# Kernel tuning notes

Hardware: AMD Instinct MI355X
Metric: run time of the kernel (lower is better)

The kernel has to match this reference:

```python
import jax, jax.numpy as jnp
import numpy as np

B, S, M, KD, VD, QD, H, NQ = 256, 200, 32, 128, 256, 128, 64, 10000
TA, TB, TC = 0.075, 0.088, 1.0  # triangular membership params a, b, c


def setup_inputs() -> dict:
    key = jax.random.key(0)
    ks = jax.random.split(key, 12)
    q_data = jax.random.randint(ks[0], (B, S), 0, NQ + 1)
    # kaiming-normal-ish embedding table; padding_idx=0 row zeroed
    q_embed_weight = jax.random.normal(ks[1], (NQ + 1, QD)) * np.sqrt(2.0 / QD)
    q_embed_weight = q_embed_weight.at[0].set(0.0)
    key_mem = jax.random.normal(ks[2], (M, KD)) * np.sqrt(2.0 / KD)
    value_mem = jax.random.normal(ks[3], (M, VD)) * np.sqrt(2.0 / VD)
    in_dim = VD + QD
    s = 1.0 / np.sqrt(H)
    W_ih = jax.random.uniform(ks[4], (4 * H, in_dim), minval=-s, maxval=s)
    W_hh = jax.random.uniform(ks[5], (4 * H, H), minval=-s, maxval=s)
    b_ih = jax.random.uniform(ks[6], (4 * H,), minval=-s, maxval=s)
    b_hh = jax.random.uniform(ks[7], (4 * H,), minval=-s, maxval=s)
    W_pred = jax.random.normal(ks[8], (1, H)) * np.sqrt(2.0 / H)
    b_pred = jnp.zeros((1,))
    init_h = jax.random.normal(ks[9], (B, H))
    init_c = jax.random.normal(ks[10], (B, H))
    return dict(q_data=q_data, q_embed_weight=q_embed_weight, key_mem=key_mem,
                value_mem=value_mem, W_ih=W_ih, W_hh=W_hh, b_ih=b_ih, b_hh=b_hh,
                W_pred=W_pred, b_pred=b_pred, init_h=init_h, init_c=init_c)


def triangular_layer(cw):
    """cw: [N, M] correlation weights -> [N] unique-row indices.
    Faithful to torch: trit-quantize each weight {0,1,2}, then map each row to its
    index in the (lexicographically sorted) unique-row table, which is exactly what
    the pairwise squared-distance matmul + (dist==0).nonzero() trick computes."""
    w = jnp.minimum((cw - TA) / (TB - TA), (TC - cw) / (TC - TB))
    w = jnp.maximum(w, 0.0)
    iv = jnp.where(w >= 0.6, 2, jnp.where(w >= 0.1, 1, 0)).astype(jnp.int32)  # [N, M]
    # pack 32 trits into two int32 keys (3^16 < 2^31)
    p = jnp.power(3, jnp.arange(16, dtype=jnp.int32))  # [16]
    kh = (iv[:, :16] * p).sum(1)
    kl = (iv[:, 16:] * p).sum(1)
    order = jnp.lexsort((kl, kh))  # primary key kh
    kh_s, kl_s = kh[order], kl[order]
    change = jnp.concatenate([jnp.zeros((1,), jnp.int32),
                              ((kh_s[1:] != kh_s[:-1]) | (kl_s[1:] != kl_s[:-1])).astype(jnp.int32)])
    rank_sorted = jnp.cumsum(change)
    inv = jnp.zeros(cw.shape[0], jnp.int32).at[order].set(rank_sorted)
    return inv


def reference(q_data, q_embed_weight, key_mem, value_mem, W_ih, W_hh, b_ih, b_hh,
              W_pred, b_pred, init_h, init_c):
    q_emb = q_embed_weight[q_data]                                  # [B,S,QD]
    cw = jax.nn.softmax(jnp.einsum('bsd,md->bsm', q_emb, key_mem))  # DKVMN attention
    read = jnp.einsum('bsm,mv->bsv', cw, value_mem)                 # [B,S,VD]
    ids = triangular_layer(cw.reshape(B * S, M))                    # [B*S]
    x = jnp.concatenate([read, q_emb], axis=-1)                     # [B,S,VD+QD]

    def step(carry, xt):
        h, c = carry
        g = xt @ W_ih.T + h @ W_hh.T + b_ih + b_hh
        i, f, gg, o = jnp.split(g, 4, axis=-1)
        c = jax.nn.sigmoid(f) * c + jax.nn.sigmoid(i) * jnp.tanh(gg)
        h = jax.nn.sigmoid(o) * jnp.tanh(c)
        return (h, c), h

    _, hs = jax.lax.scan(step, (init_h, init_c), jnp.swapaxes(x, 0, 1))
    hs = jnp.swapaxes(hs, 0, 1)                                     # [B,S,H]
    pred = jax.nn.sigmoid(hs @ W_pred.T + b_pred)[..., 0]           # [B,S]
    return pred, ids
```

## Files before the change

kernel.cpp:

```cpp
#include <hip/hip_runtime.h>

#define BB 256
#define SS 200
#define MM 32
#define KDIM 128
#define VDIM 256
#define QDIM 128
#define HH 64
#define NROWS 10001
#define NSAMP (BB*SS)
#define INDIM (VDIM+QDIM)
#define DHS 8192
#define DHMASK (DHS-1)
#define XR 16
#define NB_ATTN 2501

typedef unsigned long long u64;
typedef unsigned int u32;
typedef float f16v __attribute__((ext_vector_type(16)));

__device__ __forceinline__ float fexp(float x){ return __builtin_amdgcn_exp2f(x * 1.44269504f); }
__device__ __forceinline__ float fsigm(float x){ return __builtin_amdgcn_rcpf(1.f + fexp(-x)); }
__device__ __forceinline__ float ftanh(float x){ return 1.f - 2.f*__builtin_amdgcn_rcpf(1.f + fexp(2.f*x)); }
__device__ __forceinline__ int clampq(int q){ return q < 0 ? 0 : (q > NROWS-1 ? NROWS-1 : q); }

__device__ __forceinline__ u32 hash64(u64 x){
  x ^= x >> 33; x *= 0xff51afd7ed558ccdULL;
  x ^= x >> 33; x *= 0xc4ceb9fe1a85ec53ULL;
  x ^= x >> 33;
  return (u32)x;
}

__device__ __forceinline__ u64 shflx64(u64 v, int m){
  int lo = __shfl_xor((int)(u32)v, m, 64);
  int hi = __shfl_xor((int)(u32)(v >> 32), m, 64);
  return ((u64)(u32)hi << 32) | (u32)lo;
}

__global__ void k_tr(const float* __restrict__ W_ih, const float* __restrict__ key_mem,
                     float* __restrict__ WQT4, float* __restrict__ KT,
                     float* __restrict__ WVT, u32* __restrict__ present){
  int idx = blockIdx.x*256 + threadIdx.x;
  if (idx < 131072) {
    int dd = idx & 3, j = (idx >> 2) & 255, d4 = idx >> 10;
    WQT4[idx] = W_ih[j*INDIM + VDIM + 4*d4 + dd];
  } else if (idx < 135168) {
    int t = idx - 131072;
    int m = t & 31, d = t >> 5; KT[t] = key_mem[m*KDIM + d];
  } else if (idx < 200704) {
    int t = idx - 135168;
    int j = t & 255, v = t >> 8; WVT[v*256 + j] = W_ih[j*INDIM + v];
  } else {
    int t = idx - 200704;
    if (t < NROWS) present[t] = 0u;
  }
}

__global__ __launch_bounds__(256) void k_front(
    const float* __restrict__ emb, const float* __restrict__ KT,
    const float* __restrict__ val, const float* __restrict__ WVT,
    const int* __restrict__ q_data,
    float* __restrict__ CW, u64* __restrict__ KEYT,
    float* __restrict__ VW, u32* __restrict__ present){
  int bid = blockIdx.x;
  if (bid < NB_ATTN) {
    int w = threadIdx.x >> 6, l = threadIdx.x & 63;
    int n = bid*4 + w;
    __shared__ float se[4][QDIM];
    bool valid = (n < NROWS);
    if (valid) {
      se[w][l]      = emb[n*QDIM + l];
      se[w][l + 64] = emb[n*QDIM + l + 64];
    }
    __syncthreads();
    int m = l & 31;
    float logit = 0.f;
    if (valid && l < 32)
      for (int d = 0; d < KDIM; ++d) logit += se[w][d] * KT[d*32 + m];
    float mx = logit;
    #pragma unroll
    for (int msk = 16; msk >= 1; msk >>= 1) mx = fmaxf(mx, __shfl_xor(mx, msk, 64));
    float e = (l < 32) ? expf(logit - mx) : 0.f;
    float sum = e;
    #pragma unroll
    for (int msk = 16; msk >= 1; msk >>= 1) sum += __shfl_xor(sum, msk, 64);
    float cw = e / sum;
    float wv = fminf((cw - 0.075f)/0.013f, (1.0f - cw)/0.912f);
    wv = fmaxf(wv, 0.f);
    int iv = (wv >= 0.6f) ? 2 : ((wv >= 0.1f) ? 1 : 0);
    int ee = (m < 16) ? m + 16 : m - 16;
    u64 p3 = 1;
    for (int i = 0; i < 31; ++i) if (i < ee) p3 *= 3ULL;
    u64 term = (valid && l < 32) ? (u64)iv * p3 : 0ULL;
    #pragma unroll
    for (int msk = 16; msk >= 1; msk >>= 1) term += shflx64(term, msk);
    if (valid && l < 32) CW[n*256 + m] = cw;
    if (valid && l == 0) KEYT[n] = term;
  } else if (bid < NB_ATTN + MM) {
    int m = bid - NB_ATTN, j = threadIdx.x;
    __shared__ float sval[VDIM];
    sval[j] = val[m*VDIM + j];
    __syncthreads();
    float a0=0.f, a1=0.f, a2=0.f, a3=0.f;
    for (int v = 0; v < VDIM; v += 4) {
      a0 += sval[v+0]*WVT[(v+0)*256 + j];
      a1 += sval[v+1]*WVT[(v+1)*256 + j];
      a2 += sval[v+2]*WVT[(v+2)*256 + j];
      a3 += sval[v+3]*WVT[(v+3)*256 + j];
    }
    VW[m*256 + j] = (a0+a1)+(a2+a3);
  } else {
    int i = (bid - NB_ATTN - MM)*256 + threadIdx.x;
    if (i < NSAMP) present[clampq(q_data[i])] = 1u;
  }
}

__global__ __launch_bounds__(256) void k_xw(
    const float* __restrict__ CW, const float* __restrict__ emb,
    const float* __restrict__ VW, const float* __restrict__ WQT4,
    const float* __restrict__ b_ih, const float* __restrict__ b_hh,
    float* __restrict__ XW4){
  int base = blockIdx.x * XR;
  int j = threadIdx.x;
  __shared__ float scw[XR][32];
  __shared__ __align__(16) float ses[XR][QDIM];
  for (int idx = j; idx < XR*32; idx += 256) {
    int r = idx >> 5, m = idx & 31, n = base + r;
    scw[r][m] = (n < NROWS) ? CW[n*256 + m] : 0.f;
  }
  for (int idx = j; idx < XR*QDIM; idx += 256) {
    int r = idx >> 7, d = idx & 127, n = base + r;
    ses[r][d] = (n < NROWS) ? emb[n*QDIM + d] : 0.f;
  }
  __syncthreads();
  float bias = b_ih[j] + b_hh[j];
  float acc[XR];
  #pragma unroll
  for (int r = 0; r < XR; ++r) acc[r] = bias;
  for (int m = 0; m < MM; ++m) {
    float wv = VW[m*256 + j];
    #pragma unroll
    for (int r = 0; r < XR; ++r) acc[r] += scw[r][m] * wv;
  }
  for (int d4 = 0; d4 < QDIM/4; ++d4) {
    float4 wq = *(const float4*)(WQT4 + d4*1024 + j*4);
    #pragma unroll
    for (int r = 0; r < XR; ++r) {
      float4 ev = *(const float4*)(&ses[r][4*d4]);
      acc[r] += ev.x*wq.x + ev.y*wq.y + ev.z*wq.z + ev.w*wq.w;
    }
  }
  int gate = j >> 6, unit = j & 63;
  #pragma unroll
  for (int r = 0; r < XR; ++r)
    if (base + r < NROWS) XW4[(size_t)(base + r)*256 + 4*unit + gate] = acc[r];
}

__global__ __launch_bounds__(1024) void k_dedup(
    const u32* __restrict__ present, const u64* __restrict__ KEYT,
    u32* __restrict__ g_htab, u32* __restrict__ g_pay,
    u32* __restrict__ counter, u64* __restrict__ uniq){
  __shared__ u32 sh_tab[DHS];
  __shared__ u32 sh_pay[DHS];
  __shared__ u32 sh_cnt;
  int tid = threadIdx.x;
  for (int i = tid; i < DHS; i += 1024) sh_tab[i] = 0u;
  if (tid == 0) sh_cnt = 0u;
  __syncthreads();
  for (int n = tid; n < NROWS; n += 1024) {
    if (present[n] != 1u) continue;
    u64 key = KEYT[n];
    u32 h = hash64(key) & DHMASK;
    while (true) {
      u32 cur = sh_tab[h];
      if (cur != 0u) {
        if (KEYT[cur-1u] == key) break;
        h = (h + 1) & DHMASK; continue;
      }
      u32 prev = atomicCAS(&sh_tab[h], 0u, (u32)(n + 1));
      if (prev == 0u) {
        u32 idx = atomicAdd(&sh_cnt, 1u);
        uniq[idx] = key;
        sh_pay[h] = idx;
        break;
      }
      if (KEYT[prev-1u] == key) break;
      h = (h + 1) & DHMASK;
    }
  }
  __syncthreads();
  for (int i = tid; i < DHS; i += 1024) {
    u32 v = sh_tab[i];
    g_htab[i] = v;
    g_pay[i]  = v ? sh_pay[i] : 0u;
  }
  if (tid == 0) *counter = sh_cnt;
}

__global__ __launch_bounds__(256) void k_rank(const u64* __restrict__ uniq,
                                              const u32* __restrict__ counter,
                                              u32* __restrict__ RANK){
  __shared__ u64 chunk[2048];
  u32 U = *counter;
  int u = blockIdx.x*256 + threadIdx.x;
  u64 mykey = (u < (int)U) ? uniq[u] : 0;
  u32 cnt = 0;
  for (u32 base = 0; base < U; base += 2048) {
    u32 n = (U - base < 2048u) ? (U - base) : 2048u;
    __syncthreads();
    for (u32 t = threadIdx.x; t < n; t += 256) chunk[t] = uniq[base + t];
    __syncthreads();
    if (u < (int)U)
      for (u32 j = 0; j < n; ++j) cnt += (chunk[j] < mykey) ? 1u : 0u;
  }
  if (u < (int)U) RANK[u] = cnt;
}

__global__ void k_qrank(const u32* __restrict__ present, const u64* __restrict__ KEYT,
                        const u32* __restrict__ g_htab, const u32* __restrict__ g_pay,
                        const u32* __restrict__ RANK, u32* __restrict__ RANKQ){
  int n = blockIdx.x*blockDim.x + threadIdx.x;
  if (n >= NROWS || present[n] != 1u) return;
  u64 key = KEYT[n];
  u32 h = hash64(key) & DHMASK;
  while (true) {
    u32 cur = g_htab[h];
    if (cur != 0u && KEYT[cur-1u] == key) { RANKQ[n] = RANK[g_pay[h]]; return; }
    h = (h + 1) & DHMASK;
  }
}

__global__ void k_ids(const int* __restrict__ q_data, const u32* __restrict__ RANKQ,
                      float* __restrict__ out_ids){
  int i = blockIdx.x*blockDim.x + threadIdx.x;
  if (i >= NSAMP) return;
  out_ids[i] = (float)RANKQ[clampq(q_data[i])];
}

#define DOT16(acc, W, H) do { \
  acc += (W)[0]*(H)[0];   acc += (W)[1]*(H)[1];   acc += (W)[2]*(H)[2];   acc += (W)[3]*(H)[3]; \
  acc += (W)[4]*(H)[4];   acc += (W)[5]*(H)[5];   acc += (W)[6]*(H)[6];   acc += (W)[7]*(H)[7]; \
  acc += (W)[8]*(H)[8];   acc += (W)[9]*(H)[9];   acc += (W)[10]*(H)[10]; acc += (W)[11]*(H)[11]; \
  acc += (W)[12]*(H)[12]; acc += (W)[13]*(H)[13]; acc += (W)[14]*(H)[14]; acc += (W)[15]*(H)[15]; \
} while(0)

__global__ __launch_bounds__(256, 1) void k_lstm(
    const int* __restrict__ q_data, const float* __restrict__ XW4,
    const float* __restrict__ W_hh,
    const float* __restrict__ W_pred, const float* __restrict__ b_pred,
    const float* __restrict__ init_h, const float* __restrict__ init_c,
    float* __restrict__ out_pred){
  const int b = blockIdx.x;
  const int t = threadIdx.x;
  const int w = t >> 6, l = t & 63;
  const int uo = l & 15, k = l >> 4;
  const int u = 16*w + uo;
  __shared__ __align__(64) float Hbuf[SS][64];
  __shared__ int   sq[SS];
  __shared__ float swp[HH];

  for (int s = t; s < SS; s += 256) sq[s] = clampq(q_data[b*SS + s]);
  if (t < HH) swp[t] = W_pred[t];

  const float* wb = W_hh + (size_t)u*HH + 16*k;
  f16v Wi = *(const f16v*)(wb +     0);
  f16v Wf = *(const f16v*)(wb +  4096);
  f16v Wg = *(const f16v*)(wb +  8192);
  f16v Wo = *(const f16v*)(wb + 12288);

  f16v H = *(const f16v*)(init_h + (size_t)b*HH + 16*k);
  float c  = init_c[b*HH + u];
  float bp = b_pred[0];
  __syncthreads();

  float4 xwA = *(const float4*)(XW4 + (size_t)sq[0]*256 + 4*u);
  float4 xwB = *(const float4*)(XW4 + (size_t)sq[1]*256 + 4*u);

  for (int s = 0; s < SS; ++s) {
    int sp = (s + 2 < SS) ? s + 2 : SS - 1;
    float4 xwC = *(const float4*)(XW4 + (size_t)sq[sp]*256 + 4*u);
    float pi=0.f, pf=0.f, pg=0.f, po=0.f;
    DOT16(pi, Wi, H); DOT16(pf, Wf, H); DOT16(pg, Wg, H); DOT16(po, Wo, H);
    pi += __shfl_xor(pi, 16, 64); pf += __shfl_xor(pf, 16, 64);
    pg += __shfl_xor(pg, 16, 64); po += __shfl_xor(po, 16, 64);
    pi += __shfl_xor(pi, 32, 64); pf += __shfl_xor(pf, 32, 64);
    pg += __shfl_xor(pg, 32, 64); po += __shfl_xor(po, 32, 64);
    float ai = xwA.x + pi;
    float af = xwA.y + pf;
    float ag = xwA.z + pg;
    float ao = xwA.w + po;
    c = fsigm(af)*c + fsigm(ai)*ftanh(ag);
    float hh = fsigm(ao)*ftanh(c);
    if (l < 16) Hbuf[s][u] = hh;
    __syncthreads();
    H = *(const f16v*)(&Hbuf[s][16*k]);
    xwA = xwB; xwB = xwC;
  }
  __syncthreads();

  for (int s = t; s < SS; s += 256) {
    float acc = 0.f;
    #pragma unroll 16
    for (int kk = 0; kk < HH; ++kk) {
      int k2 = (kk + t) & 63;
      acc += Hbuf[s][k2] * swp[k2];
    }
    out_pred[b*SS + s] = fsigm(acc + bp);
  }
}

extern "C" void kernel_launch(void* const* d_in, const int* in_sizes, int n_in,
                              void* d_out, int out_size, void* d_ws, size_t ws_size,
                              hipStream_t stream) {
  const int*   q_data  = (const int*)d_in[0];
  const float* emb     = (const float*)d_in[1];
  const float* keym    = (const float*)d_in[2];
  const float* val     = (const float*)d_in[3];
  const float* W_ih    = (const float*)d_in[4];
  const float* W_hh    = (const float*)d_in[5];
  const float* b_ih    = (const float*)d_in[6];
  const float* b_hh    = (const float*)d_in[7];
  const float* W_pred  = (const float*)d_in[8];
  const float* b_pred  = (const float*)d_in[9];
  const float* init_h  = (const float*)d_in[10];
  const float* init_c  = (const float*)d_in[11];

  char* ws = (char*)d_ws;
  float* XW4     = (float*)(ws + 0);
  float* VW      = (float*)(ws + 10241024);
  u64*  KEYT     = (u64*) (ws + 10273792);
  u64*  uniq     = (u64*) (ws + 10353920);
  u32*  RANK     = (u32*) (ws + 10434048);
  u32*  g_htab   = (u32*) (ws + 10474240);
  u32*  g_pay    = (u32*) (ws + 10507008);
  u32*  counter  = (u32*) (ws + 10539776);
  u32*  present  = (u32*) (ws + 10539840);
  u32*  RANKQ    = (u32*) (ws + 10579904);
  float* WQT4    = (float*)(ws + 10619968);
  float* KT      = (float*)(ws + 11144256);
  float* WVT     = (float*)(ws + 11160640);
  float* CW      = XW4;

  float* out_pred = (float*)d_out;
  float* out_ids  = out_pred + NSAMP;

  hipLaunchKernelGGL(k_tr,    dim3(824), dim3(256), 0, stream,
                     W_ih, keym, WQT4, KT, WVT, present);
  hipLaunchKernelGGL(k_front, dim3(NB_ATTN + MM + 200), dim3(256), 0, stream,
                     emb, KT, val, WVT, q_data, CW, KEYT, VW, present);
  hipLaunchKernelGGL(k_dedup, dim3(1), dim3(1024), 0, stream,
                     present, KEYT, g_htab, g_pay, counter, uniq);
  hipLaunchKernelGGL(k_rank,  dim3((NROWS+255)/256), dim3(256), 0, stream, uniq, counter, RANK);
  hipLaunchKernelGGL(k_qrank, dim3((NROWS+255)/256), dim3(256), 0, stream,
                     present, KEYT, g_htab, g_pay, RANK, RANKQ);
  hipLaunchKernelGGL(k_xw,    dim3((NROWS+XR-1)/XR), dim3(256), 0, stream,
                     CW, emb, VW, WQT4, b_ih, b_hh, XW4);
  hipLaunchKernelGGL(k_ids,   dim3((NSAMP+255)/256), dim3(256), 0, stream, q_data, RANKQ, out_ids);
  hipLaunchKernelGGL(k_lstm,  dim3(BB), dim3(256), 0, stream,
                     q_data, XW4, W_hh, W_pred, b_pred, init_h, init_c, out_pred);
}
```

Measured before the change: 239.7 us.

## Run LSTM recurrence in a single wave using readlane broadcasts, no barriers

The LSTM kernel now uses one 64-thread wave per batch row, so each thread owns one hidden unit. The hidden state is broadcast across lanes with readlane instead of going through shared memory, which removes the per-step block barrier and the cross-lane shuffle reductions. The i/f gate rows of W_hh stay in registers, while the g/o rows are staged in LDS in an interleaved layout and read as float4 every step. The cost is a sequential 64-term dot product per gate per thread, scalar readlane traffic, and heavy register pressure, with only one wave per block.

New measurement: 403.5 us. 68.3% more time.

```diff
diff --git a/kernel.cpp b/kernel.cpp
--- a/kernel.cpp
+++ b/kernel.cpp
@@ -17,7 +17,6 @@
 
 typedef unsigned long long u64;
 typedef unsigned int u32;
-typedef float f16v __attribute__((ext_vector_type(16)));
 
 __device__ __forceinline__ float fexp(float x){ return __builtin_amdgcn_exp2f(x * 1.44269504f); }
 __device__ __forceinline__ float fsigm(float x){ return __builtin_amdgcn_rcpf(1.f + fexp(-x)); }
@@ -237,14 +236,36 @@
   out_ids[i] = (float)RANKQ[clampq(q_data[i])];
 }
 
-#define DOT16(acc, W, H) do { \
-  acc += (W)[0]*(H)[0];   acc += (W)[1]*(H)[1];   acc += (W)[2]*(H)[2];   acc += (W)[3]*(H)[3]; \
-  acc += (W)[4]*(H)[4];   acc += (W)[5]*(H)[5];   acc += (W)[6]*(H)[6];   acc += (W)[7]*(H)[7]; \
-  acc += (W)[8]*(H)[8];   acc += (W)[9]*(H)[9];   acc += (W)[10]*(H)[10]; acc += (W)[11]*(H)[11]; \
-  acc += (W)[12]*(H)[12]; acc += (W)[13]*(H)[13]; acc += (W)[14]*(H)[14]; acc += (W)[15]*(H)[15]; \
-} while(0)
-
-__global__ __launch_bounds__(256, 1) void k_lstm(
+#define PINV(v4) asm volatile("" : "+v"((v4).x), "+v"((v4).y), "+v"((v4).z), "+v"((v4).w))
+
+#define RLF(j) __int_as_float(__builtin_amdgcn_readlane(hb, (j)))
+
+#define STEP4(WI, WF, G, O, j0, PI, PF, PG, PO) do{ \
+  float h0=RLF((j0)+0), h1=RLF((j0)+1), h2=RLF((j0)+2), h3=RLF((j0)+3); \
+  PI += (WI).x*h0; PF += (WF).x*h0; PG += (G).x*h0; PO += (O).x*h0; \
+  PI += (WI).y*h1; PF += (WF).y*h1; PG += (G).y*h1; PO += (O).y*h1; \
+  PI += (WI).z*h2; PF += (WF).z*h2; PG += (G).z*h2; PO += (O).z*h2; \
+  PI += (WI).w*h3; PF += (WF).w*h3; PG += (G).w*h3; PO += (O).w*h3; \
+}while(0)
+
+#define QTR(q, A0,A1,A2,A3, F0,F1,F2,F3, PI,PF,PG,PO) do{ \
+  float4 G0 = *(const float4*)(WGO + og + (4*(q)+0)*256 + 4*u); \
+  float4 G1 = *(const float4*)(WGO + og + (4*(q)+1)*256 + 4*u); \
+  float4 G2 = *(const float4*)(WGO + og + (4*(q)+2)*256 + 4*u); \
+  float4 G3 = *(const float4*)(WGO + og + (4*(q)+3)*256 + 4*u); \
+  float4 Q0 = *(const float4*)(WGO + og + 4096 + (4*(q)+0)*256 + 4*u); \
+  float4 Q1 = *(const float4*)(WGO + og + 4096 + (4*(q)+1)*256 + 4*u); \
+  float4 Q2 = *(const float4*)(WGO + og + 4096 + (4*(q)+2)*256 + 4*u); \
+  float4 Q3 = *(const float4*)(WGO + og + 4096 + (4*(q)+3)*256 + 4*u); \
+  STEP4(A0,F0,G0,Q0, 16*(q)+0,  PI,PF,PG,PO); \
+  STEP4(A1,F1,G1,Q1, 16*(q)+4,  PI,PF,PG,PO); \
+  STEP4(A2,F2,G2,Q2, 16*(q)+8,  PI,PF,PG,PO); \
+  STEP4(A3,F3,G3,Q3, 16*(q)+12, PI,PF,PG,PO); \
+}while(0)
+
+__global__ __launch_bounds__(64)
+__attribute__((amdgpu_waves_per_eu(1, 1)))
+void k_lstm(
     const int* __restrict__ q_data, const float* __restrict__ XW4,
     const float* __restrict__ W_hh,
     const float* __restrict__ W_pred, const float* __restrict__ b_pred,
@@ -252,25 +273,50 @@
     float* __restrict__ out_pred){
   const int b = blockIdx.x;
   const int t = threadIdx.x;
-  const int w = t >> 6, l = t & 63;
-  const int uo = l & 15, k = l >> 4;
-  const int u = 16*w + uo;
+  const int u = t;
   __shared__ __align__(64) float Hbuf[SS][64];
+  __shared__ float WGO[8192];
   __shared__ int   sq[SS];
   __shared__ float swp[HH];
 
-  for (int s = t; s < SS; s += 256) sq[s] = clampq(q_data[b*SS + s]);
-  if (t < HH) swp[t] = W_pred[t];
-
-  const float* wb = W_hh + (size_t)u*HH + 16*k;
-  f16v Wi = *(const f16v*)(wb +     0);
-  f16v Wf = *(const f16v*)(wb +  4096);
-  f16v Wg = *(const f16v*)(wb +  8192);
-  f16v Wo = *(const f16v*)(wb + 12288);
-
-  f16v H = *(const f16v*)(init_h + (size_t)b*HH + 16*k);
-  float c  = init_c[b*HH + u];
-  float bp = b_pred[0];
+  for (int s = t; s < SS; s += 64) sq[s] = clampq(q_data[b*SS + s]);
+  swp[t] = W_pred[t];
+  for (int i = t; i < 4096; i += 64) {
+    int dd = i & 3, uu = (i >> 2) & 63, j4 = i >> 8;
+    WGO[i]        = W_hh[(size_t)(2*HH + uu)*HH + 4*j4 + dd];
+    WGO[4096 + i] = W_hh[(size_t)(3*HH + uu)*HH + 4*j4 + dd];
+  }
+
+  const float* wbi = W_hh + (size_t)u*HH;
+  const float* wbf = W_hh + (size_t)(HH + u)*HH;
+  float4 wi00=*(const float4*)(wbi+ 0), wi01=*(const float4*)(wbi+ 4);
+  float4 wi02=*(const float4*)(wbi+ 8), wi03=*(const float4*)(wbi+12);
+  float4 wi04=*(const float4*)(wbi+16), wi05=*(const float4*)(wbi+20);
+  float4 wi06=*(const float4*)(wbi+24), wi07=*(const float4*)(wbi+28);
+  float4 wi08=*(const float4*)(wbi+32), wi09=*(const float4*)(wbi+36);
+  float4 wi10=*(const float4*)(wbi+40), wi11=*(const float4*)(wbi+44);
+  float4 wi12=*(const float4*)(wbi+48), wi13=*(const float4*)(wbi+52);
+  float4 wi14=*(const float4*)(wbi+56), wi15=*(const float4*)(wbi+60);
+  float4 wf00=*(const float4*)(wbf+ 0), wf01=*(const float4*)(wbf+ 4);
+  float4 wf02=*(const float4*)(wbf+ 8), wf03=*(const float4*)(wbf+12);
+  float4 wf04=*(const float4*)(wbf+16), wf05=*(const float4*)(wbf+20);
+  float4 wf06=*(const float4*)(wbf+24), wf07=*(const float4*)(wbf+28);
+  float4 wf08=*(const float4*)(wbf+32), wf09=*(const float4*)(wbf+36);
+  float4 wf10=*(const float4*)(wbf+40), wf11=*(const float4*)(wbf+44);
+  float4 wf12=*(const float4*)(wbf+48), wf13=*(const float4*)(wbf+52);
+  float4 wf14=*(const float4*)(wbf+56), wf15=*(const float4*)(wbf+60);
+  PINV(wi00); PINV(wi01); PINV(wi02); PINV(wi03);
+  PINV(wi04); PINV(wi05); PINV(wi06); PINV(wi07);
+  PINV(wi08); PINV(wi09); PINV(wi10); PINV(wi11);
+  PINV(wi12); PINV(wi13); PINV(wi14); PINV(wi15);
+  PINV(wf00); PINV(wf01); PINV(wf02); PINV(wf03);
+  PINV(wf04); PINV(wf05); PINV(wf06); PINV(wf07);
+  PINV(wf08); PINV(wf09); PINV(wf10); PINV(wf11);
+  PINV(wf12); PINV(wf13); PINV(wf14); PINV(wf15);
+
+  float hval = init_h[b*HH + u];
+  float c    = init_c[b*HH + u];
+  float bp   = b_pred[0];
   __syncthreads();
 
   float4 xwA = *(const float4*)(XW4 + (size_t)sq[0]*256 + 4*u);
@@ -279,26 +325,29 @@
   for (int s = 0; s < SS; ++s) {
     int sp = (s + 2 < SS) ? s + 2 : SS - 1;
     float4 xwC = *(const float4*)(XW4 + (size_t)sq[sp]*256 + 4*u);
-    float pi=0.f, pf=0.f, pg=0.f, po=0.f;
-    DOT16(pi, Wi, H); DOT16(pf, Wf, H); DOT16(pg, Wg, H); DOT16(po, Wo, H);
-    pi += __shfl_xor(pi, 16, 64); pf += __shfl_xor(pf, 16, 64);
-    pg += __shfl_xor(pg, 16, 64); po += __shfl_xor(po, 16, 64);
-    pi += __shfl_xor(pi, 32, 64); pf += __shfl_xor(pf, 32, 64);
-    pg += __shfl_xor(pg, 32, 64); po += __shfl_xor(po, 32, 64);
-    float ai = xwA.x + pi;
-    float af = xwA.y + pf;
-    float ag = xwA.z + pg;
-    float ao = xwA.w + po;
+    int og = 0; asm volatile("" : "+v"(og));
+    int hb = __float_as_int(hval);
+    float PI0=0.f,PF0=0.f,PG0=0.f,PO0=0.f;
+    float PI1=0.f,PF1=0.f,PG1=0.f,PO1=0.f;
+    float PI2=0.f,PF2=0.f,PG2=0.f,PO2=0.f;
+    float PI3=0.f,PF3=0.f,PG3=0.f,PO3=0.f;
+    QTR(0, wi00,wi01,wi02,wi03, wf00,wf01,wf02,wf03, PI0,PF0,PG0,PO0);
+    QTR(1, wi04,wi05,wi06,wi07, wf04,wf05,wf06,wf07, PI1,PF1,PG1,PO1);
+    QTR(2, wi08,wi09,wi10,wi11, wf08,wf09,wf10,wf11, PI2,PF2,PG2,PO2);
+    QTR(3, wi12,wi13,wi14,wi15, wf12,wf13,wf14,wf15, PI3,PF3,PG3,PO3);
+    float ai = xwA.x + ((PI0+PI1)+(PI2+PI3));
+    float af = xwA.y + ((PF0+PF1)+(PF2+PF3));
+    float ag = xwA.z + ((PG0+PG1)+(PG2+PG3));
+    float ao = xwA.w + ((PO0+PO1)+(PO2+PO3));
     c = fsigm(af)*c + fsigm(ai)*ftanh(ag);
     float hh = fsigm(ao)*ftanh(c);
-    if (l < 16) Hbuf[s][u] = hh;
-    __syncthreads();
-    H = *(const f16v*)(&Hbuf[s][16*k]);
+    Hbuf[s][u] = hh;
+    hval = hh;
     xwA = xwB; xwB = xwC;
   }
   __syncthreads();
 
-  for (int s = t; s < SS; s += 256) {
+  for (int s = t; s < SS; s += 64) {
     float acc = 0.f;
     #pragma unroll 16
     for (int kk = 0; kk < HH; ++kk) {
@@ -356,6 +405,6 @@
   hipLaunchKernelGGL(k_xw,    dim3((NROWS+XR-1)/XR), dim3(256), 0, stream,
                      CW, emb, VW, WQT4, b_ih, b_hh, XW4);
   hipLaunchKernelGGL(k_ids,   dim3((NSAMP+255)/256), dim3(256), 0, stream, q_data, RANKQ, out_ids);
-  hipLaunchKernelGGL(k_lstm,  dim3(BB), dim3(256), 0, stream,
+  hipLaunchKernelGGL(k_lstm,  dim3(BB), dim3(64), 0, stream,
                      q_data, XW4, W_hh, W_pred, b_pred, init_h, init_c, out_pred);
 }
```

## Fuse dedup, rank, qrank and ids into one cooperative grid-synced kernel

Applied to the files above, without the earlier changes.

Replaces the single-block shared-memory dedup kernel and three follow-on launches with one cooperative kernel of 40 blocks. The hash table moves to global memory with grid-wide syncs between phases. The goal is to cut launch overhead and the serial single-block hashing. In exchange it adds grid.sync costs, global-memory atomics and a cooperative-launch path.

Result: slower. 364.4 us (+52.0%).

```diff
diff --git a/kernel.cpp b/kernel.cpp
--- a/kernel.cpp
+++ b/kernel.cpp
@@ -1,4 +1,7 @@
 #include <hip/hip_runtime.h>
+#include <hip/hip_cooperative_groups.h>
+
+namespace cg = cooperative_groups;
 
 #define BB 256
 #define SS 200
@@ -14,6 +17,7 @@
 #define DHMASK (DHS-1)
 #define XR 16
 #define NB_ATTN 2501
+#define TB 40
 
 typedef unsigned long long u64;
 typedef unsigned int u32;
@@ -23,6 +27,13 @@
 __device__ __forceinline__ float fsigm(float x){ return __builtin_amdgcn_rcpf(1.f + fexp(-x)); }
 __device__ __forceinline__ float ftanh(float x){ return 1.f - 2.f*__builtin_amdgcn_rcpf(1.f + fexp(2.f*x)); }
 __device__ __forceinline__ int clampq(int q){ return q < 0 ? 0 : (q > NROWS-1 ? NROWS-1 : q); }
+
+__device__ __forceinline__ u32 lda32(const u32* p){
+  return __hip_atomic_load(p, __ATOMIC_RELAXED, __HIP_MEMORY_SCOPE_AGENT);
+}
+__device__ __forceinline__ u64 lda64(const u64* p){
+  return __hip_atomic_load(p, __ATOMIC_RELAXED, __HIP_MEMORY_SCOPE_AGENT);
+}
 
 __device__ __forceinline__ u32 hash64(u64 x){
   x ^= x >> 33; x *= 0xff51afd7ed558ccdULL;
@@ -156,85 +167,69 @@
     if (base + r < NROWS) XW4[(size_t)(base + r)*256 + 4*unit + gate] = acc[r];
 }
 
-__global__ __launch_bounds__(1024) void k_dedup(
+__global__ __launch_bounds__(256) void k_tail(
     const u32* __restrict__ present, const u64* __restrict__ KEYT,
+    const int* __restrict__ q_data,
     u32* __restrict__ g_htab, u32* __restrict__ g_pay,
-    u32* __restrict__ counter, u64* __restrict__ uniq){
-  __shared__ u32 sh_tab[DHS];
-  __shared__ u32 sh_pay[DHS];
-  __shared__ u32 sh_cnt;
-  int tid = threadIdx.x;
-  for (int i = tid; i < DHS; i += 1024) sh_tab[i] = 0u;
-  if (tid == 0) sh_cnt = 0u;
-  __syncthreads();
-  for (int n = tid; n < NROWS; n += 1024) {
-    if (present[n] != 1u) continue;
+    u32* __restrict__ counter, u64* __restrict__ uniq,
+    u32* __restrict__ RANK, u32* __restrict__ RANKQ,
+    float* __restrict__ out_ids){
+  cg::grid_group grid = cg::this_grid();
+  const int gtid = blockIdx.x*256 + threadIdx.x;
+  const int n = gtid;
+  for (int i = gtid; i < DHS; i += TB*256) g_htab[i] = 0u;
+  if (gtid == 0) *counter = 0u;
+  grid.sync();
+  if (n < NROWS && present[n] == 1u) {
     u64 key = KEYT[n];
     u32 h = hash64(key) & DHMASK;
     while (true) {
-      u32 cur = sh_tab[h];
+      u32 cur = lda32(&g_htab[h]);
       if (cur != 0u) {
         if (KEYT[cur-1u] == key) break;
         h = (h + 1) & DHMASK; continue;
       }
-      u32 prev = atomicCAS(&sh_tab[h], 0u, (u32)(n + 1));
+      u32 prev = atomicCAS(&g_htab[h], 0u, (u32)(n + 1));
       if (prev == 0u) {
-        u32 idx = atomicAdd(&sh_cnt, 1u);
+        u32 idx = atomicAdd(counter, 1u);
         uniq[idx] = key;
-        sh_pay[h] = idx;
+        g_pay[h] = idx;
         break;
       }
       if (KEYT[prev-1u] == key) break;
       h = (h + 1) & DHMASK;
     }
   }
-  __syncthreads();
-  for (int i = tid; i < DHS; i += 1024) {
-    u32 v = sh_tab[i];
-    g_htab[i] = v;
-    g_pay[i]  = v ? sh_pay[i] : 0u;
-  }
-  if (tid == 0) *counter = sh_cnt;
-}
-
-__global__ __launch_bounds__(256) void k_rank(const u64* __restrict__ uniq,
-                                              const u32* __restrict__ counter,
-                                              u32* __restrict__ RANK){
+  grid.sync();
+  u32 U = lda32(counter);
   __shared__ u64 chunk[2048];
-  u32 U = *counter;
-  int u = blockIdx.x*256 + threadIdx.x;
-  u64 mykey = (u < (int)U) ? uniq[u] : 0;
+  u64 mykey = (gtid < (int)U) ? lda64(&uniq[gtid]) : 0;
   u32 cnt = 0;
   for (u32 base = 0; base < U; base += 2048) {
-    u32 n = (U - base < 2048u) ? (U - base) : 2048u;
-    __syncthreads();
-    for (u32 t = threadIdx.x; t < n; t += 256) chunk[t] = uniq[base + t];
-    __syncthreads();
-    if (u < (int)U)
-      for (u32 j = 0; j < n; ++j) cnt += (chunk[j] < mykey) ? 1u : 0u;
-  }
-  if (u < (int)U) RANK[u] = cnt;
-}
-
-__global__ void k_qrank(const u32* __restrict__ present, const u64* __restrict__ KEYT,
-                        const u32* __restrict__ g_htab, const u32* __restrict__ g_pay,
-                        const u32* __restrict__ RANK, u32* __restrict__ RANKQ){
-  int n = blockIdx.x*blockDim.x + threadIdx.x;
-  if (n >= NROWS || present[n] != 1u) return;
-  u64 key = KEYT[n];
-  u32 h = hash64(key) & DHMASK;
-  while (true) {
-    u32 cur = g_htab[h];
-    if (cur != 0u && KEYT[cur-1u] == key) { RANKQ[n] = RANK[g_pay[h]]; return; }
-    h = (h + 1) & DHMASK;
-  }
-}
-
-__global__ void k_ids(const int* __restrict__ q_data, const u32* __restrict__ RANKQ,
-                      float* __restrict__ out_ids){
-  int i = blockIdx.x*blockDim.x + threadIdx.x;
-  if (i >= NSAMP) return;
-  out_ids[i] = (float)RANKQ[clampq(q_data[i])];
+    u32 nn = (U - base < 2048u) ? (U - base) : 2048u;
+    __syncthreads();
+    for (u32 tt = threadIdx.x; tt < nn; tt += 256) chunk[tt] = lda64(&uniq[base + tt]);
+    __syncthreads();
+    if (gtid < (int)U)
+      for (u32 j = 0; j < nn; ++j) cnt += (chunk[j] < mykey) ? 1u : 0u;
+  }
+  if (gtid < (int)U) RANK[gtid] = cnt;
+  grid.sync();
+  if (n < NROWS && present[n] == 1u) {
+    u64 key = KEYT[n];
+    u32 h = hash64(key) & DHMASK;
+    while (true) {
+      u32 cur = lda32(&g_htab[h]);
+      if (cur != 0u && KEYT[cur-1u] == key) {
+        RANKQ[n] = lda32(&RANK[lda32(&g_pay[h])]);
+        break;
+      }
+      h = (h + 1) & DHMASK;
+    }
+  }
+  grid.sync();
+  for (int i = gtid; i < NSAMP; i += TB*256)
+    out_ids[i] = (float)lda32(&RANKQ[clampq(q_data[i])]);
 }
 
 #define DOT16(acc, W, H) do { \
@@ -348,14 +343,15 @@
                      W_ih, keym, WQT4, KT, WVT, present);
   hipLaunchKernelGGL(k_front, dim3(NB_ATTN + MM + 200), dim3(256), 0, stream,
                      emb, KT, val, WVT, q_data, CW, KEYT, VW, present);
-  hipLaunchKernelGGL(k_dedup, dim3(1), dim3(1024), 0, stream,
-                     present, KEYT, g_htab, g_pay, counter, uniq);
-  hipLaunchKernelGGL(k_rank,  dim3((NROWS+255)/256), dim3(256), 0, stream, uniq, counter, RANK);
-  hipLaunchKernelGGL(k_qrank, dim3((NROWS+255)/256), dim3(256), 0, stream,
-                     present, KEYT, g_htab, g_pay, RANK, RANKQ);
   hipLaunchKernelGGL(k_xw,    dim3((NROWS+XR-1)/XR), dim3(256), 0, stream,
                      CW, emb, VW, WQT4, b_ih, b_hh, XW4);
-  hipLaunchKernelGGL(k_ids,   dim3((NSAMP+255)/256), dim3(256), 0, stream, q_data, RANKQ, out_ids);
+  {
+    void* targs[] = { (void*)&present, (void*)&KEYT, (void*)&q_data,
+                      (void*)&g_htab, (void*)&g_pay, (void*)&counter,
+                      (void*)&uniq, (void*)&RANK, (void*)&RANKQ,
+                      (void*)&out_ids };
+    hipLaunchCooperativeKernel((void*)k_tail, dim3(TB), dim3(256), targs, 0, stream);
+  }
   hipLaunchKernelGGL(k_lstm,  dim3(BB), dim3(256), 0, stream,
                      q_data, XW4, W_hh, W_pred, b_pred, init_h, init_c, out_pred);
 }
```
